# Kernel optimization log

Measured on AMD Instinct MI355X. Metric: run time of the kernel, lower is better.

## Reference

```python
import jax, jax.numpy as jnp
import numpy as np

N = 8192
COUP = 0.08
ALPHA = 0.45
DT = 0.01
DIFF = 10.0


def setup_inputs() -> dict:
    key = jax.random.key(0)
    k1, k2, k3 = jax.random.split(key, 3)
    phase = jax.random.normal(k1, (N,), dtype=jnp.float32)
    w = jax.random.uniform(k2, (N,), dtype=jnp.float32) * (2.0 * np.pi * 1.5)
    xy = jax.random.normal(k3, (N, 2), dtype=jnp.float32) * 0.05
    xy_dot_old = jnp.zeros((N, 2), dtype=jnp.float32)
    return {"phase": phase, "w": w, "xy": xy, "xy_dot_old": xy_dot_old}


def reference(phase, w, xy, xy_dot_old):
    n = xy.shape[0]
    x = xy[:, 0]
    y = xy[:, 1]

    # per-edge rotation R(d_ij) with d_ij = phase_i - phase_j; diagonal d_ii = 0 -> R = I
    d = phase[:, None] - phase[None, :]            # (n, n)
    c = jnp.cos(d)
    s = jnp.sin(d)

    # sum_j R_ij @ xy_j over ALL j (diagonal contributes identity * xy_i),
    # then remove the self term since adjacency excludes i == j.
    sum_x = c @ x - s @ y                          # (n,)
    sum_y = s @ x + c @ y
    inv_deg = 1.0 / (n - 1)
    coup_x = COUP * (sum_x - x) * inv_deg
    coup_y = COUP * (sum_y - y) * inv_deg

    # local Hopf-like dynamics
    r2 = x * x + y * y
    a = ALPHA * (1.0 - r2)
    xdot = a * x - w * y + coup_x
    ydot = w * x + a * y + coup_y

    # slew-rate clamp to old derivative +/- DIFF
    xdot = jnp.clip(xdot, xy_dot_old[:, 0] - DIFF, xy_dot_old[:, 0] + DIFF)
    ydot = jnp.clip(ydot, xy_dot_old[:, 1] - DIFF, xy_dot_old[:, 1] + DIFF)

    new_xyd = jnp.stack([xdot, ydot], axis=-1)     # (n, 2)
    new_xy = xy + DT * new_xyd                     # (n, 2)
    y_unit = jnp.clip(new_xy[:, 1], -1.0, 1.0)     # unit outputs in [-1, 1]
    return new_xy, new_xyd, y_unit
```

## Files before the change

### kernel.cpp

```cpp
#include <hip/hip_runtime.h>
#include <math.h>


#define NOSC 8192
#define NTHR 128
#define NBLK (NOSC / NTHR)

__global__ __launch_bounds__(NTHR, 1) void nacpg_partial(
    const float* __restrict__ phase,
    const float* __restrict__ xy,
    float4* __restrict__ part)
{
    const int i = blockIdx.x * NTHR + threadIdx.x;
    const float p = phase[i];
    const float2 v = reinterpret_cast<const float2*>(xy)[i];
    float s, c;
    __sincosf(p, &s, &c);

    float A = c * v.x;
    float B = s * v.x;
    float C = c * v.y;
    float D = s * v.y;

    #pragma unroll
    for (int off = 32; off >= 1; off >>= 1) {
        A += __shfl_xor(A, off);
        B += __shfl_xor(B, off);
        C += __shfl_xor(C, off);
        D += __shfl_xor(D, off);
    }

    __shared__ float4 red[NTHR / 64];
    const int wave = threadIdx.x >> 6;
    const int lane = threadIdx.x & 63;
    if (lane == 0) red[wave] = make_float4(A, B, C, D);
    __syncthreads();
    if (threadIdx.x == 0) {
        float4 a = red[0], b = red[1];
        part[blockIdx.x] = make_float4(a.x + b.x, a.y + b.y, a.z + b.z, a.w + b.w);
    }
}

__global__ __launch_bounds__(NTHR, 1) void nacpg_main(
    const float* __restrict__ phase,
    const float* __restrict__ w,
    const float* __restrict__ xy,
    const float* __restrict__ xy_dot_old,
    const float4* __restrict__ part,
    float* __restrict__ out)
{
    constexpr float COUP  = 0.08f;
    constexpr float ALPHA = 0.45f;
    constexpr float DT    = 0.01f;
    constexpr float DIFF  = 10.0f;

    const int i    = blockIdx.x * NTHR + threadIdx.x;
    const int lane = threadIdx.x & 63;

    const float p       = phase[i];
    const float wi      = w[i];
    const float2 v      = reinterpret_cast<const float2*>(xy)[i];
    const float2 old    = reinterpret_cast<const float2*>(xy_dot_old)[i];

    float4 pp = part[lane];
    float A = pp.x, B = pp.y, C = pp.z, D = pp.w;
    #pragma unroll
    for (int off = 32; off >= 1; off >>= 1) {
        A += __shfl_xor(A, off);
        B += __shfl_xor(B, off);
        C += __shfl_xor(C, off);
        D += __shfl_xor(D, off);
    }

    const float AD = A + D;
    const float BC = B - C;
    const float CB = C - B;
    const float inv_deg = 1.0f / (float)(NOSC - 1);

    float s, c;
    __sincosf(p, &s, &c);

    const float xi = v.x, yi = v.y;
    const float sum_x = c * AD + s * BC;
    const float sum_y = s * AD + c * CB;
    const float coup_x = COUP * (sum_x - xi) * inv_deg;
    const float coup_y = COUP * (sum_y - yi) * inv_deg;

    const float r2 = xi * xi + yi * yi;
    const float a  = ALPHA * (1.0f - r2);

    float xdot = a * xi - wi * yi + coup_x;
    float ydot = wi * xi + a * yi + coup_y;

    xdot = fminf(fmaxf(xdot, old.x - DIFF), old.x + DIFF);
    ydot = fminf(fmaxf(ydot, old.y - DIFF), old.y + DIFF);

    const float nx = xi + DT * xdot;
    const float ny = yi + DT * ydot;

    reinterpret_cast<float2*>(out)[i]             = make_float2(nx, ny);
    reinterpret_cast<float2*>(out + 2 * NOSC)[i]  = make_float2(xdot, ydot);
    out[4 * NOSC + i] = fminf(fmaxf(ny, -1.0f), 1.0f);
}

extern "C" void kernel_launch(void* const* d_in, const int* in_sizes, int n_in,
                              void* d_out, int out_size, void* d_ws, size_t ws_size,
                              hipStream_t stream) {
    const float* phase      = (const float*)d_in[0];
    const float* w          = (const float*)d_in[1];
    const float* xy         = (const float*)d_in[2];
    const float* xy_dot_old = (const float*)d_in[3];
    float* out   = (float*)d_out;
    float4* part = (float4*)d_ws;

    nacpg_partial<<<NBLK, NTHR, 0, stream>>>(phase, xy, part);
    nacpg_main<<<NBLK, NTHR, 0, stream>>>(phase, w, xy, xy_dot_old, part, out);
}
```

Measured before the change: 61.34 us.

## Fuse partial reduction and main pass into one kernel with redundant per-block reduction

Replaces the two-kernel scheme (per-block partial sums written to workspace, then a second kernel reducing them) with a single kernel. Each of 64 blocks redundantly computes the full global sums A,B,C,D over all 8192 oscillators using vectorized float4 loads, then handles its own 128 outputs. This removes one kernel launch and the global workspace round trip, but every block now performs all 8192 sincos evaluations instead of a slice.

```diff
diff --git a/kernel.cpp b/kernel.cpp
--- a/kernel.cpp
+++ b/kernel.cpp
@@ -3,24 +3,49 @@
 
 
 #define NOSC 8192
-#define NTHR 128
-#define NBLK (NOSC / NTHR)
+#define NTHR 256
+#define NBLK 64
+#define EPB  (NOSC / NBLK)
 
-__global__ __launch_bounds__(NTHR, 1) void nacpg_partial(
+__global__ __launch_bounds__(NTHR, 1) void nacpg_fused(
     const float* __restrict__ phase,
+    const float* __restrict__ w,
     const float* __restrict__ xy,
-    float4* __restrict__ part)
+    const float* __restrict__ xy_dot_old,
+    float* __restrict__ out)
 {
-    const int i = blockIdx.x * NTHR + threadIdx.x;
-    const float p = phase[i];
-    const float2 v = reinterpret_cast<const float2*>(xy)[i];
-    float s, c;
-    __sincosf(p, &s, &c);
+    constexpr float COUP  = 0.08f;
+    constexpr float ALPHA = 0.45f;
+    constexpr float DT    = 0.01f;
+    constexpr float DIFF  = 10.0f;
 
-    float A = c * v.x;
-    float B = s * v.x;
-    float C = c * v.y;
-    float D = s * v.y;
+    const int t = threadIdx.x;
+
+    const float4* __restrict__ ph4 = reinterpret_cast<const float4*>(phase);
+    const float4* __restrict__ xy4 = reinterpret_cast<const float4*>(xy);
+
+    float A = 0.f, B = 0.f, C = 0.f, D = 0.f;
+
+    auto acc = [&](float p, float vx, float vy) {
+        float s, c;
+        __sincosf(p, &s, &c);
+        A = fmaf(c, vx, A);
+        B = fmaf(s, vx, B);
+        C = fmaf(c, vy, C);
+        D = fmaf(s, vy, D);
+    };
+
+    #pragma unroll
+    for (int k = 0; k < NOSC / 4 / NTHR; ++k) {
+        const int idx = t + k * NTHR;
+        const float4 p = ph4[idx];
+        const float4 a = xy4[2 * idx];
+        const float4 b = xy4[2 * idx + 1];
+        acc(p.x, a.x, a.y);
+        acc(p.y, a.z, a.w);
+        acc(p.z, b.x, b.y);
+        acc(p.w, b.z, b.w);
+    }
 
     #pragma unroll
     for (int off = 32; off >= 1; off >>= 1) {
@@ -31,45 +56,16 @@
     }
 
     __shared__ float4 red[NTHR / 64];
-    const int wave = threadIdx.x >> 6;
-    const int lane = threadIdx.x & 63;
+    const int wave = t >> 6;
+    const int lane = t & 63;
     if (lane == 0) red[wave] = make_float4(A, B, C, D);
     __syncthreads();
-    if (threadIdx.x == 0) {
-        float4 a = red[0], b = red[1];
-        part[blockIdx.x] = make_float4(a.x + b.x, a.y + b.y, a.z + b.z, a.w + b.w);
-    }
-}
-
-__global__ __launch_bounds__(NTHR, 1) void nacpg_main(
-    const float* __restrict__ phase,
-    const float* __restrict__ w,
-    const float* __restrict__ xy,
-    const float* __restrict__ xy_dot_old,
-    const float4* __restrict__ part,
-    float* __restrict__ out)
-{
-    constexpr float COUP  = 0.08f;
-    constexpr float ALPHA = 0.45f;
-    constexpr float DT    = 0.01f;
-    constexpr float DIFF  = 10.0f;
-
-    const int i    = blockIdx.x * NTHR + threadIdx.x;
-    const int lane = threadIdx.x & 63;
-
-    const float p       = phase[i];
-    const float wi      = w[i];
-    const float2 v      = reinterpret_cast<const float2*>(xy)[i];
-    const float2 old    = reinterpret_cast<const float2*>(xy_dot_old)[i];
-
-    float4 pp = part[lane];
-    float A = pp.x, B = pp.y, C = pp.z, D = pp.w;
-    #pragma unroll
-    for (int off = 32; off >= 1; off >>= 1) {
-        A += __shfl_xor(A, off);
-        B += __shfl_xor(B, off);
-        C += __shfl_xor(C, off);
-        D += __shfl_xor(D, off);
+    {
+        const float4 r0 = red[0], r1 = red[1], r2 = red[2], r3 = red[3];
+        A = r0.x + r1.x + r2.x + r3.x;
+        B = r0.y + r1.y + r2.y + r3.y;
+        C = r0.z + r1.z + r2.z + r3.z;
+        D = r0.w + r1.w + r2.w + r3.w;
     }
 
     const float AD = A + D;
@@ -77,30 +73,39 @@
     const float CB = C - B;
     const float inv_deg = 1.0f / (float)(NOSC - 1);
 
-    float s, c;
-    __sincosf(p, &s, &c);
+    if (t < EPB) {
+        const int i = blockIdx.x * EPB + t;
 
-    const float xi = v.x, yi = v.y;
-    const float sum_x = c * AD + s * BC;
-    const float sum_y = s * AD + c * CB;
-    const float coup_x = COUP * (sum_x - xi) * inv_deg;
-    const float coup_y = COUP * (sum_y - yi) * inv_deg;
+        const float p    = phase[i];
+        const float wi   = w[i];
+        const float2 v   = reinterpret_cast<const float2*>(xy)[i];
+        const float2 old = reinterpret_cast<const float2*>(xy_dot_old)[i];
 
-    const float r2 = xi * xi + yi * yi;
-    const float a  = ALPHA * (1.0f - r2);
+        float s, c;
+        __sincosf(p, &s, &c);
 
-    float xdot = a * xi - wi * yi + coup_x;
-    float ydot = wi * xi + a * yi + coup_y;
+        const float xi = v.x, yi = v.y;
+        const float sum_x = c * AD + s * BC;
+        const float sum_y = s * AD + c * CB;
+        const float coup_x = COUP * (sum_x - xi) * inv_deg;
+        const float coup_y = COUP * (sum_y - yi) * inv_deg;
 
-    xdot = fminf(fmaxf(xdot, old.x - DIFF), old.x + DIFF);
-    ydot = fminf(fmaxf(ydot, old.y - DIFF), old.y + DIFF);
+        const float r2 = xi * xi + yi * yi;
+        const float a  = ALPHA * (1.0f - r2);
 
-    const float nx = xi + DT * xdot;
-    const float ny = yi + DT * ydot;
+        float xdot = a * xi - wi * yi + coup_x;
+        float ydot = wi * xi + a * yi + coup_y;
 
-    reinterpret_cast<float2*>(out)[i]             = make_float2(nx, ny);
-    reinterpret_cast<float2*>(out + 2 * NOSC)[i]  = make_float2(xdot, ydot);
-    out[4 * NOSC + i] = fminf(fmaxf(ny, -1.0f), 1.0f);
+        xdot = fminf(fmaxf(xdot, old.x - DIFF), old.x + DIFF);
+        ydot = fminf(fmaxf(ydot, old.y - DIFF), old.y + DIFF);
+
+        const float nx = xi + DT * xdot;
+        const float ny = yi + DT * ydot;
+
+        reinterpret_cast<float2*>(out)[i]            = make_float2(nx, ny);
+        reinterpret_cast<float2*>(out + 2 * NOSC)[i] = make_float2(xdot, ydot);
+        out[4 * NOSC + i] = fminf(fmaxf(ny, -1.0f), 1.0f);
+    }
 }
 
 extern "C" void kernel_launch(void* const* d_in, const int* in_sizes, int n_in,
@@ -110,9 +115,7 @@
     const float* w          = (const float*)d_in[1];
     const float* xy         = (const float*)d_in[2];
     const float* xy_dot_old = (const float*)d_in[3];
-    float* out   = (float*)d_out;
-    float4* part = (float4*)d_ws;
+    float* out = (float*)d_out;
 
-    nacpg_partial<<<NBLK, NTHR, 0, stream>>>(phase, xy, part);
-    nacpg_main<<<NBLK, NTHR, 0, stream>>>(phase, w, xy, xy_dot_old, part, out);
+    nacpg_fused<<<NBLK, NTHR, 0, stream>>>(phase, w, xy, xy_dot_old, out);
 }
```

Result: no change. 60.41 us (-1.5%).
